# Kernel tuning notes

Measured on AMD Instinct MI355X. Metric: run time of the kernel, lower is better.

Reference implementation:

```python
import jax, jax.numpy as jnp
import numpy as np

N, E = 8192, 65536
IN_C, OUT_C, EF = 64, 16, 8
L1, L2 = 48, 32  # in - floor((in-out)/3), in - floor(2*(in-out)/3)


def setup_inputs() -> dict:
    key = jax.random.key(0)
    ks = jax.random.split(key, 10)
    rn = lambda k, shape, s: jax.random.normal(k, shape, dtype=jnp.float32) * s
    return {
        "x": jax.random.normal(ks[0], (N, IN_C), dtype=jnp.float32),
        "edge_index": jax.random.randint(ks[1], (2, E), 0, N, dtype=jnp.int32),
        "edge_attr": jax.random.normal(ks[2], (E, EF), dtype=jnp.float32),
        "nn1_w": rn(ks[3], (EF, IN_C * L1), 0.05),
        "nn1_b": jnp.zeros((IN_C * L1,), jnp.float32),
        "root1": rn(ks[4], (IN_C, L1), 0.1),
        "bias1": jnp.zeros((L1,), jnp.float32),
        "nn2_w": rn(ks[5], (EF, L1 * L2), 0.05),
        "nn2_b": jnp.zeros((L1 * L2,), jnp.float32),
        "root2": rn(ks[6], (L1, L2), 0.1),
        "bias2": jnp.zeros((L2,), jnp.float32),
        "mu_w": rn(ks[7], (L2, OUT_C), 0.1),
        "mu_b": jnp.zeros((OUT_C,), jnp.float32),
        "ls_w": rn(ks[8], (L2, OUT_C), 0.1),
        "ls_b": jnp.zeros((OUT_C,), jnp.float32),
    }


def _nnconv(x, src, dst, edge_attr, nn_w, nn_b, root, bias, c_in, c_out):
    # edge MLP -> per-edge weight matrices [E, c_in, c_out]
    w = (edge_attr @ nn_w + nn_b).reshape(-1, c_in, c_out)
    msg = jnp.einsum('ei,eio->eo', x[src], w)  # gather + per-edge matvec
    agg = jax.ops.segment_sum(msg, dst, num_segments=x.shape[0])  # sum aggregation
    return agg + x @ root + bias  # root transform + bias


def _gcn(x, src, dst, w, b):
    n = x.shape[0]
    # degree over target nodes, including self-loop (edge_weight = 1)
    deg = jax.ops.segment_sum(jnp.ones_like(src, jnp.float32), dst, num_segments=n) + 1.0
    dinv = jax.lax.rsqrt(deg)
    h = x @ w
    norm = dinv[src] * dinv[dst]  # [E]
    agg = jax.ops.segment_sum(h[src] * norm[:, None], dst, num_segments=n)
    return agg + h * (1.0 / deg)[:, None] + b  # self-loop contribution: deg_i^{-1}


def reference(x, edge_index, edge_attr, nn1_w, nn1_b, root1, bias1,
              nn2_w, nn2_b, root2, bias2, mu_w, mu_b, ls_w, ls_b):
    src, dst = edge_index[0], edge_index[1]
    h = jax.nn.relu(_nnconv(x, src, dst, edge_attr, nn1_w, nn1_b, root1, bias1, IN_C, L1))
    h = jax.nn.relu(_nnconv(h, src, dst, edge_attr, nn2_w, nn2_b, root2, bias2, L1, L2))
    return (_gcn(h, src, dst, mu_w, mu_b), _gcn(h, src, dst, ls_w, ls_b))
```

## Files before the change

kernel.cpp:

```cpp
#include <hip/hip_runtime.h>

#define NN 8192
#define EE 65536
#define IN_C 64
#define L1C 48
#define L2C 32
#define OUT_C 16
#define EF 8

#define T1_COLS 480
#define T2_COLS 320

__global__ __launch_bounds__(256) void k_T1(const float* __restrict__ x,
                                            const float* __restrict__ w,
                                            const float* __restrict__ b,
                                            const float* __restrict__ root,
                                            float* __restrict__ T1) {
    __shared__ float xsT[64 * 16];
    const int n0 = blockIdx.x * 16;
    for (int t = threadIdx.x; t < 16 * 64; t += 256) {
        int n = t >> 6, i = t & 63;
        xsT[i * 16 + n] = x[(n0 + n) * 64 + i];
    }
    __syncthreads();
    for (int c = threadIdx.x; c < T1_COLS; c += 256) {
        int f = c / 48, o = c - f * 48;
        const float* wp;
        if (f < 8)      wp = w + f * 3072 + o;
        else if (f == 8) wp = b + o;
        else             wp = root + o;
        float acc[16];
#pragma unroll
        for (int n = 0; n < 16; n++) acc[n] = 0.f;
#pragma unroll 16
        for (int i = 0; i < 64; i++) {
            float wv = wp[i * 48];
            const float* xr = &xsT[i * 16];
#pragma unroll
            for (int n = 0; n < 16; n++) acc[n] += xr[n] * wv;
        }
#pragma unroll
        for (int n = 0; n < 16; n++) T1[(size_t)(n0 + n) * T1_COLS + c] = acc[n];
    }
}

__global__ __launch_bounds__(256) void k_T2(const float* __restrict__ h1,
                                            const float* __restrict__ w,
                                            const float* __restrict__ b,
                                            const float* __restrict__ root,
                                            float* __restrict__ T2) {
    __shared__ float xsT[48 * 16];
    const int n0 = blockIdx.x * 16;
    for (int t = threadIdx.x; t < 16 * 48; t += 256) {
        int n = t / 48, i = t - n * 48;
        xsT[i * 16 + n] = h1[(n0 + n) * 48 + i];
    }
    __syncthreads();
    for (int c = threadIdx.x; c < T2_COLS; c += 256) {
        int f = c >> 5, o = c & 31;
        const float* wp;
        if (f < 8)      wp = w + f * 1536 + o;
        else if (f == 8) wp = b + o;
        else             wp = root + o;
        float acc[16];
#pragma unroll
        for (int n = 0; n < 16; n++) acc[n] = 0.f;
#pragma unroll 16
        for (int i = 0; i < 48; i++) {
            float wv = wp[i * 32];
            const float* xr = &xsT[i * 16];
#pragma unroll
            for (int n = 0; n < 16; n++) acc[n] += xr[n] * wv;
        }
#pragma unroll
        for (int n = 0; n < 16; n++) T2[(size_t)(n0 + n) * T2_COLS + c] = acc[n];
    }
}

__global__ __launch_bounds__(256) void k_zero(float* __restrict__ p, int n4) {
    int i = blockIdx.x * 256 + threadIdx.x;
    if (i < n4) ((float4*)p)[i] = make_float4(0.f, 0.f, 0.f, 0.f);
}

__global__ __launch_bounds__(256) void k_count(const int* __restrict__ ei,
                                               int* __restrict__ cnt) {
    int e = blockIdx.x * 256 + threadIdx.x;
    if (e < EE) atomicAdd(&cnt[ei[EE + e]], 1);
}

__global__ __launch_bounds__(256) void k_scan(const int* __restrict__ cnt,
                                              int* __restrict__ rowstart,
                                              int* __restrict__ cursor) {
    __shared__ int part[256];
    const int t = threadIdx.x;
    const int base = t * 32;
    int local[32];
    int sum = 0;
#pragma unroll
    for (int k = 0; k < 32; k++) { local[k] = cnt[base + k]; sum += local[k]; }
    part[t] = sum;
    __syncthreads();
    if (t == 0) {
        int run = 0;
        for (int i = 0; i < 256; i++) { int c = part[i]; part[i] = run; run += c; }
    }
    __syncthreads();
    int run = part[t];
#pragma unroll
    for (int k = 0; k < 32; k++) {
        rowstart[base + k] = run;
        cursor[base + k] = run;
        run += local[k];
    }
    if (t == 255) rowstart[8192] = run;
}

__global__ __launch_bounds__(256) void k_scatter(const int* __restrict__ ei,
                                                 int* __restrict__ cursor,
                                                 int* __restrict__ ssrc,
                                                 int* __restrict__ seid) {
    int e = blockIdx.x * 256 + threadIdx.x;
    if (e >= EE) return;
    int d = ei[EE + e];
    int pos = atomicAdd(&cursor[d], 1);
    ssrc[pos] = ei[e];
    seid[pos] = e;
}

__global__ __launch_bounds__(256) void k_agg1(const int* __restrict__ rowstart,
                                              const int* __restrict__ ssrc,
                                              const int* __restrict__ seid,
                                              const float* __restrict__ ea,
                                              const float* __restrict__ T1,
                                              const float* __restrict__ bias1,
                                              float* __restrict__ h1) {
    int idx = blockIdx.x * 256 + threadIdx.x;
    int n = idx / 48, o = idx - n * 48;
    if (n >= NN) return;
    const int rs = rowstart[n], re = rowstart[n + 1];
    float m = 0.f;
    for (int j = rs; j < re; ++j) {
        int s = ssrc[j], eid = seid[j];
        const float* t = T1 + (size_t)s * T1_COLS + o;
        const float4* a4 = (const float4*)(ea + (size_t)eid * 8);
        float4 a0 = a4[0], a1 = a4[1];
        float acc = t[384];
        acc += a0.x * t[0 * 48];
        acc += a0.y * t[1 * 48];
        acc += a0.z * t[2 * 48];
        acc += a0.w * t[3 * 48];
        acc += a1.x * t[4 * 48];
        acc += a1.y * t[5 * 48];
        acc += a1.z * t[6 * 48];
        acc += a1.w * t[7 * 48];
        m += acc;
    }
    float v = m + T1[(size_t)n * T1_COLS + 432 + o] + bias1[o];
    h1[(size_t)n * 48 + o] = v > 0.f ? v : 0.f;
}

__global__ __launch_bounds__(256) void k_agg2(const int* __restrict__ rowstart,
                                              const int* __restrict__ ssrc,
                                              const int* __restrict__ seid,
                                              const float* __restrict__ ea,
                                              const float* __restrict__ T2,
                                              const float* __restrict__ bias2,
                                              const float* __restrict__ mu_w,
                                              const float* __restrict__ mu_b,
                                              const float* __restrict__ ls_w,
                                              const float* __restrict__ ls_b,
                                              float* __restrict__ hmu,
                                              float* __restrict__ hls,
                                              float* __restrict__ dinv,
                                              float* __restrict__ out) {
    __shared__ float h2s[8][32];
    const int n0 = blockIdx.x * 8;
    const int lid = threadIdx.x >> 5;
    const int o = threadIdx.x & 31;
    const int n = n0 + lid;
    const int rs = rowstart[n], re = rowstart[n + 1];
    float m = 0.f;
    for (int j = rs; j < re; ++j) {
        int s = ssrc[j], eid = seid[j];
        const float* t = T2 + (size_t)s * T2_COLS + o;
        const float4* a4 = (const float4*)(ea + (size_t)eid * 8);
        float4 a0 = a4[0], a1 = a4[1];
        float acc = t[256];
        acc += a0.x * t[0 * 32];
        acc += a0.y * t[1 * 32];
        acc += a0.z * t[2 * 32];
        acc += a0.w * t[3 * 32];
        acc += a1.x * t[4 * 32];
        acc += a1.y * t[5 * 32];
        acc += a1.z * t[6 * 32];
        acc += a1.w * t[7 * 32];
        m += acc;
    }
    float v = m + T2[(size_t)n * T2_COLS + 288 + o] + bias2[o];
    h2s[lid][o] = v > 0.f ? v : 0.f;
    __syncthreads();
    const float* wm = (o < 16) ? mu_w : ls_w;
    const float* bb = (o < 16) ? mu_b : ls_b;
    const int oo = o & 15;
    float acc = 0.f;
#pragma unroll
    for (int i = 0; i < 32; i++) acc += h2s[lid][i] * wm[i * 16 + oo];
    float d = (float)(re - rs) + 1.0f;
    float di = rsqrtf(d);
    if (o == 0) dinv[n] = di;
    float init = acc / d + bb[oo];
    if (o < 16) {
        hmu[(size_t)n * 16 + oo] = acc;
        out[(size_t)n * 16 + oo] = init;
    } else {
        hls[(size_t)n * 16 + oo] = acc;
        out[(size_t)NN * 16 + (size_t)n * 16 + oo] = init;
    }
}

__global__ __launch_bounds__(256) void k_gcn(const int* __restrict__ rowstart,
                                             const int* __restrict__ ssrc,
                                             const float* __restrict__ hmu,
                                             const float* __restrict__ hls,
                                             const float* __restrict__ dinv,
                                             float* __restrict__ out) {
    int idx = blockIdx.x * 256 + threadIdx.x;
    int d = idx >> 4, o = idx & 15;
    if (d >= NN) return;
    const int rs = rowstart[d], re = rowstart[d + 1];
    float accm = 0.f, accl = 0.f;
    for (int j = rs; j < re; ++j) {
        int s = ssrc[j];
        float ds_ = dinv[s];
        accm += hmu[(size_t)s * 16 + o] * ds_;
        accl += hls[(size_t)s * 16 + o] * ds_;
    }
    float did = dinv[d];
    out[(size_t)d * 16 + o] += accm * did;
    out[(size_t)NN * 16 + (size_t)d * 16 + o] += accl * did;
}

extern "C" void kernel_launch(void* const* d_in, const int* in_sizes, int n_in,
                              void* d_out, int out_size, void* d_ws, size_t ws_size,
                              hipStream_t stream) {
    const float* x     = (const float*)d_in[0];
    const int*   ei    = (const int*)d_in[1];
    const float* ea    = (const float*)d_in[2];
    const float* nn1_w = (const float*)d_in[3];
    const float* nn1_b = (const float*)d_in[4];
    const float* root1 = (const float*)d_in[5];
    const float* bias1 = (const float*)d_in[6];
    const float* nn2_w = (const float*)d_in[7];
    const float* nn2_b = (const float*)d_in[8];
    const float* root2 = (const float*)d_in[9];
    const float* bias2 = (const float*)d_in[10];
    const float* mu_w  = (const float*)d_in[11];
    const float* mu_b  = (const float*)d_in[12];
    const float* ls_w  = (const float*)d_in[13];
    const float* ls_b  = (const float*)d_in[14];
    float* out = (float*)d_out;

    float* W    = (float*)d_ws;
    float* T1   = W;
    float* T2   = W;
    float* h1   = W + 3932160;
    float* hmu  = h1 + 393216;
    float* hls  = hmu + 131072;
    float* dinv = hls + 131072;
    int* cnt      = (int*)(dinv + 8192);
    int* rowstart = cnt + 8192;
    int* cursor   = rowstart + 8193;
    int* ssrc     = cursor + 8192;
    int* seid     = ssrc + 65536;

    k_zero<<<dim3(8), dim3(256), 0, stream>>>((float*)cnt, 2048);
    k_count<<<dim3(EE / 256), dim3(256), 0, stream>>>(ei, cnt);
    k_T1<<<dim3(NN / 16), dim3(256), 0, stream>>>(x, nn1_w, nn1_b, root1, T1);
    k_scan<<<dim3(1), dim3(256), 0, stream>>>(cnt, rowstart, cursor);
    k_scatter<<<dim3(EE / 256), dim3(256), 0, stream>>>(ei, cursor, ssrc, seid);
    k_agg1<<<dim3((NN * 48 + 255) / 256), dim3(256), 0, stream>>>(
        rowstart, ssrc, seid, ea, T1, bias1, h1);
    k_T2<<<dim3(NN / 16), dim3(256), 0, stream>>>(h1, nn2_w, nn2_b, root2, T2);
    k_agg2<<<dim3(NN / 8), dim3(256), 0, stream>>>(
        rowstart, ssrc, seid, ea, T2, bias2, mu_w, mu_b, ls_w, ls_b,
        hmu, hls, dinv, out);
    k_gcn<<<dim3((NN * 16) / 256), dim3(256), 0, stream>>>(
        rowstart, ssrc, hmu, hls, dinv, out);
}
```

Before: 175.2 us.

## Reorder NNConv math: aggregate edge-attr-weighted inputs first, then apply weights

Replaces the per-node transform tables T1/T2 (gathered per edge) with an aggregate-first formulation: each node sums ea_k * x_src over incoming edges into a Z matrix in shared memory, then one small GEMM against nn_w/nn_b/root produces the layer output. Edge attributes are permuted into CSR order during scatter, so aggregation reads them contiguously. The T1 and T2 kernels and their large workspace traffic go away, and the GCN projection is fused into layer 2. In exchange, per-block shared memory grows and the gather loops are serial per node.

```diff
diff --git a/kernel.cpp b/kernel.cpp
--- a/kernel.cpp
+++ b/kernel.cpp
@@ -2,84 +2,12 @@
 
 #define NN 8192
 #define EE 65536
-#define IN_C 64
-#define L1C 48
-#define L2C 32
-#define OUT_C 16
-#define EF 8
-
-#define T1_COLS 480
-#define T2_COLS 320
-
-__global__ __launch_bounds__(256) void k_T1(const float* __restrict__ x,
-                                            const float* __restrict__ w,
-                                            const float* __restrict__ b,
-                                            const float* __restrict__ root,
-                                            float* __restrict__ T1) {
-    __shared__ float xsT[64 * 16];
-    const int n0 = blockIdx.x * 16;
-    for (int t = threadIdx.x; t < 16 * 64; t += 256) {
-        int n = t >> 6, i = t & 63;
-        xsT[i * 16 + n] = x[(n0 + n) * 64 + i];
-    }
-    __syncthreads();
-    for (int c = threadIdx.x; c < T1_COLS; c += 256) {
-        int f = c / 48, o = c - f * 48;
-        const float* wp;
-        if (f < 8)      wp = w + f * 3072 + o;
-        else if (f == 8) wp = b + o;
-        else             wp = root + o;
-        float acc[16];
-#pragma unroll
-        for (int n = 0; n < 16; n++) acc[n] = 0.f;
-#pragma unroll 16
-        for (int i = 0; i < 64; i++) {
-            float wv = wp[i * 48];
-            const float* xr = &xsT[i * 16];
-#pragma unroll
-            for (int n = 0; n < 16; n++) acc[n] += xr[n] * wv;
-        }
-#pragma unroll
-        for (int n = 0; n < 16; n++) T1[(size_t)(n0 + n) * T1_COLS + c] = acc[n];
-    }
-}
-
-__global__ __launch_bounds__(256) void k_T2(const float* __restrict__ h1,
-                                            const float* __restrict__ w,
-                                            const float* __restrict__ b,
-                                            const float* __restrict__ root,
-                                            float* __restrict__ T2) {
-    __shared__ float xsT[48 * 16];
-    const int n0 = blockIdx.x * 16;
-    for (int t = threadIdx.x; t < 16 * 48; t += 256) {
-        int n = t / 48, i = t - n * 48;
-        xsT[i * 16 + n] = h1[(n0 + n) * 48 + i];
-    }
-    __syncthreads();
-    for (int c = threadIdx.x; c < T2_COLS; c += 256) {
-        int f = c >> 5, o = c & 31;
-        const float* wp;
-        if (f < 8)      wp = w + f * 1536 + o;
-        else if (f == 8) wp = b + o;
-        else             wp = root + o;
-        float acc[16];
-#pragma unroll
-        for (int n = 0; n < 16; n++) acc[n] = 0.f;
-#pragma unroll 16
-        for (int i = 0; i < 48; i++) {
-            float wv = wp[i * 32];
-            const float* xr = &xsT[i * 16];
-#pragma unroll
-            for (int n = 0; n < 16; n++) acc[n] += xr[n] * wv;
-        }
-#pragma unroll
-        for (int n = 0; n < 16; n++) T2[(size_t)(n0 + n) * T2_COLS + c] = acc[n];
-    }
-}
-
-__global__ __launch_bounds__(256) void k_zero(float* __restrict__ p, int n4) {
+#define ZSTRIDE 20
+
+
+__global__ __launch_bounds__(256) void k_zero(int* __restrict__ p) {
     int i = blockIdx.x * 256 + threadIdx.x;
-    if (i < n4) ((float4*)p)[i] = make_float4(0.f, 0.f, 0.f, 0.f);
+    ((int4*)p)[i] = make_int4(0, 0, 0, 0);
 }
 
 __global__ __launch_bounds__(256) void k_count(const int* __restrict__ ei,
@@ -112,109 +40,232 @@
         cursor[base + k] = run;
         run += local[k];
     }
-    if (t == 255) rowstart[8192] = run;
+    if (t == 255) rowstart[NN] = run;
 }
 
 __global__ __launch_bounds__(256) void k_scatter(const int* __restrict__ ei,
+                                                 const float* __restrict__ ea,
                                                  int* __restrict__ cursor,
                                                  int* __restrict__ ssrc,
-                                                 int* __restrict__ seid) {
+                                                 float* __restrict__ sea) {
     int e = blockIdx.x * 256 + threadIdx.x;
     if (e >= EE) return;
-    int d = ei[EE + e];
+    int s = ei[e], d = ei[EE + e];
     int pos = atomicAdd(&cursor[d], 1);
-    ssrc[pos] = ei[e];
-    seid[pos] = e;
-}
-
-__global__ __launch_bounds__(256) void k_agg1(const int* __restrict__ rowstart,
-                                              const int* __restrict__ ssrc,
-                                              const int* __restrict__ seid,
-                                              const float* __restrict__ ea,
-                                              const float* __restrict__ T1,
-                                              const float* __restrict__ bias1,
-                                              float* __restrict__ h1) {
-    int idx = blockIdx.x * 256 + threadIdx.x;
-    int n = idx / 48, o = idx - n * 48;
-    if (n >= NN) return;
-    const int rs = rowstart[n], re = rowstart[n + 1];
-    float m = 0.f;
-    for (int j = rs; j < re; ++j) {
-        int s = ssrc[j], eid = seid[j];
-        const float* t = T1 + (size_t)s * T1_COLS + o;
-        const float4* a4 = (const float4*)(ea + (size_t)eid * 8);
-        float4 a0 = a4[0], a1 = a4[1];
-        float acc = t[384];
-        acc += a0.x * t[0 * 48];
-        acc += a0.y * t[1 * 48];
-        acc += a0.z * t[2 * 48];
-        acc += a0.w * t[3 * 48];
-        acc += a1.x * t[4 * 48];
-        acc += a1.y * t[5 * 48];
-        acc += a1.z * t[6 * 48];
-        acc += a1.w * t[7 * 48];
-        m += acc;
-    }
-    float v = m + T1[(size_t)n * T1_COLS + 432 + o] + bias1[o];
-    h1[(size_t)n * 48 + o] = v > 0.f ? v : 0.f;
-}
-
-__global__ __launch_bounds__(256) void k_agg2(const int* __restrict__ rowstart,
-                                              const int* __restrict__ ssrc,
-                                              const int* __restrict__ seid,
-                                              const float* __restrict__ ea,
-                                              const float* __restrict__ T2,
-                                              const float* __restrict__ bias2,
-                                              const float* __restrict__ mu_w,
-                                              const float* __restrict__ mu_b,
-                                              const float* __restrict__ ls_w,
-                                              const float* __restrict__ ls_b,
-                                              float* __restrict__ hmu,
-                                              float* __restrict__ hls,
-                                              float* __restrict__ dinv,
-                                              float* __restrict__ out) {
-    __shared__ float h2s[8][32];
-    const int n0 = blockIdx.x * 8;
-    const int lid = threadIdx.x >> 5;
-    const int o = threadIdx.x & 31;
-    const int n = n0 + lid;
-    const int rs = rowstart[n], re = rowstart[n + 1];
-    float m = 0.f;
-    for (int j = rs; j < re; ++j) {
-        int s = ssrc[j], eid = seid[j];
-        const float* t = T2 + (size_t)s * T2_COLS + o;
-        const float4* a4 = (const float4*)(ea + (size_t)eid * 8);
-        float4 a0 = a4[0], a1 = a4[1];
-        float acc = t[256];
-        acc += a0.x * t[0 * 32];
-        acc += a0.y * t[1 * 32];
-        acc += a0.z * t[2 * 32];
-        acc += a0.w * t[3 * 32];
-        acc += a1.x * t[4 * 32];
-        acc += a1.y * t[5 * 32];
-        acc += a1.z * t[6 * 32];
-        acc += a1.w * t[7 * 32];
-        m += acc;
-    }
-    float v = m + T2[(size_t)n * T2_COLS + 288 + o] + bias2[o];
-    h2s[lid][o] = v > 0.f ? v : 0.f;
-    __syncthreads();
-    const float* wm = (o < 16) ? mu_w : ls_w;
-    const float* bb = (o < 16) ? mu_b : ls_b;
-    const int oo = o & 15;
-    float acc = 0.f;
+    ssrc[pos] = s;
+    const float4* a = (const float4*)(ea + (size_t)e * 8);
+    float4* bp = (float4*)(sea + (size_t)pos * 8);
+    bp[0] = a[0];
+    bp[1] = a[1];
+}
+
+__global__ __launch_bounds__(256) void k_L1(const int* __restrict__ rowstart,
+                                            const int* __restrict__ ssrc,
+                                            const float* __restrict__ sea,
+                                            const float* __restrict__ x,
+                                            const float* __restrict__ nn1_w,
+                                            const float* __restrict__ nn1_b,
+                                            const float* __restrict__ root1,
+                                            const float* __restrict__ bias1,
+                                            float* __restrict__ h1) {
+    __shared__ __align__(16) float Zt[640 * ZSTRIDE];
+    __shared__ float pacc[4 * 48 * 16];
+    const int n0 = blockIdx.x * 16;
+    {
+        const int g = threadIdx.x >> 6;
+        const int i = threadIdx.x & 63;
+        for (int nb = 0; nb < 16; nb += 4) {
+            const int nn = nb + g;
+            const int n = n0 + nn;
+            const int rs = rowstart[n], re = rowstart[n + 1];
+            float a0 = 0, a1 = 0, a2 = 0, a3 = 0, a4 = 0, a5 = 0, a6 = 0, a7 = 0, as = 0;
+            for (int j = rs; j < re; ++j) {
+                int s = ssrc[j];
+                float xv = x[(size_t)s * 64 + i];
+                const float4* q4 = (const float4*)(sea + (size_t)j * 8);
+                float4 e0 = q4[0], e1 = q4[1];
+                a0 += e0.x * xv; a1 += e0.y * xv; a2 += e0.z * xv; a3 += e0.w * xv;
+                a4 += e1.x * xv; a5 += e1.y * xv; a6 += e1.z * xv; a7 += e1.w * xv;
+                as += xv;
+            }
+            Zt[(0 * 64 + i) * ZSTRIDE + nn] = a0;
+            Zt[(1 * 64 + i) * ZSTRIDE + nn] = a1;
+            Zt[(2 * 64 + i) * ZSTRIDE + nn] = a2;
+            Zt[(3 * 64 + i) * ZSTRIDE + nn] = a3;
+            Zt[(4 * 64 + i) * ZSTRIDE + nn] = a4;
+            Zt[(5 * 64 + i) * ZSTRIDE + nn] = a5;
+            Zt[(6 * 64 + i) * ZSTRIDE + nn] = a6;
+            Zt[(7 * 64 + i) * ZSTRIDE + nn] = a7;
+            Zt[(512 + i) * ZSTRIDE + nn] = as;
+            Zt[(576 + i) * ZSTRIDE + nn] = x[(size_t)n * 64 + i];
+        }
+    }
+    __syncthreads();
+    {
+        const int o = threadIdx.x & 15;
+        const int q = (threadIdx.x >> 4) & 3;
+        const int ks = threadIdx.x >> 6;
+        const int k0 = ks * 160, k1 = k0 + 160;
+        float4 c0 = {0, 0, 0, 0}, c1 = {0, 0, 0, 0}, c2 = {0, 0, 0, 0};
+        const int zb = q * 4;
+        int ka1 = k1 < 512 ? k1 : 512;
+        for (int k = k0; k < ka1; ++k) {
+            const float* wp = nn1_w + k * 48 + o;
+            float w0 = wp[0], w1 = wp[16], w2 = wp[32];
+            float4 z = *(const float4*)&Zt[k * ZSTRIDE + zb];
+            c0.x += z.x * w0; c0.y += z.y * w0; c0.z += z.z * w0; c0.w += z.w * w0;
+            c1.x += z.x * w1; c1.y += z.y * w1; c1.z += z.z * w1; c1.w += z.w * w1;
+            c2.x += z.x * w2; c2.y += z.y * w2; c2.z += z.z * w2; c2.w += z.w * w2;
+        }
+        int kb0 = k0 > 512 ? k0 : 512, kb1 = k1 < 576 ? k1 : 576;
+        for (int k = kb0; k < kb1; ++k) {
+            const float* wp = nn1_b + (k - 512) * 48 + o;
+            float w0 = wp[0], w1 = wp[16], w2 = wp[32];
+            float4 z = *(const float4*)&Zt[k * ZSTRIDE + zb];
+            c0.x += z.x * w0; c0.y += z.y * w0; c0.z += z.z * w0; c0.w += z.w * w0;
+            c1.x += z.x * w1; c1.y += z.y * w1; c1.z += z.z * w1; c1.w += z.w * w1;
+            c2.x += z.x * w2; c2.y += z.y * w2; c2.z += z.z * w2; c2.w += z.w * w2;
+        }
+        int kc0 = k0 > 576 ? k0 : 576;
+        for (int k = kc0; k < k1; ++k) {
+            const float* wp = root1 + (k - 576) * 48 + o;
+            float w0 = wp[0], w1 = wp[16], w2 = wp[32];
+            float4 z = *(const float4*)&Zt[k * ZSTRIDE + zb];
+            c0.x += z.x * w0; c0.y += z.y * w0; c0.z += z.z * w0; c0.w += z.w * w0;
+            c1.x += z.x * w1; c1.y += z.y * w1; c1.z += z.z * w1; c1.w += z.w * w1;
+            c2.x += z.x * w2; c2.y += z.y * w2; c2.z += z.z * w2; c2.w += z.w * w2;
+        }
+        float* pp = pacc + (ks * 48 + o) * 16 + zb;
+        pp[0] = c0.x; pp[1] = c0.y; pp[2] = c0.z; pp[3] = c0.w;
+        pp = pacc + (ks * 48 + o + 16) * 16 + zb;
+        pp[0] = c1.x; pp[1] = c1.y; pp[2] = c1.z; pp[3] = c1.w;
+        pp = pacc + (ks * 48 + o + 32) * 16 + zb;
+        pp[0] = c2.x; pp[1] = c2.y; pp[2] = c2.z; pp[3] = c2.w;
+    }
+    __syncthreads();
+    for (int r = threadIdx.x; r < 768; r += 256) {
+        int o = r >> 4, n = r & 15;
+        float v = pacc[(0 * 48 + o) * 16 + n] + pacc[(1 * 48 + o) * 16 + n] +
+                  pacc[(2 * 48 + o) * 16 + n] + pacc[(3 * 48 + o) * 16 + n] + bias1[o];
+        h1[(size_t)(n0 + n) * 48 + o] = v > 0.f ? v : 0.f;
+    }
+}
+
+__global__ __launch_bounds__(256) void k_L2(const int* __restrict__ rowstart,
+                                            const int* __restrict__ ssrc,
+                                            const float* __restrict__ sea,
+                                            const float* __restrict__ h1,
+                                            const float* __restrict__ nn2_w,
+                                            const float* __restrict__ nn2_b,
+                                            const float* __restrict__ root2,
+                                            const float* __restrict__ bias2,
+                                            const float* __restrict__ mu_w,
+                                            const float* __restrict__ mu_b,
+                                            const float* __restrict__ ls_w,
+                                            const float* __restrict__ ls_b,
+                                            const int* __restrict__ cnt,
+                                            float* __restrict__ hmu,
+                                            float* __restrict__ hls,
+                                            float* __restrict__ dinv,
+                                            float* __restrict__ out) {
+    __shared__ __align__(16) float Zt[480 * ZSTRIDE];
+    __shared__ float pacc[4 * 32 * 16];
+    __shared__ float h2s[16 * 33];
+    const int n0 = blockIdx.x * 16;
+    {
+        const int g = threadIdx.x >> 6;
+        const int i = threadIdx.x & 63;
+        for (int nb = 0; nb < 16; nb += 4) {
+            const int nn = nb + g;
+            const int n = n0 + nn;
+            if (i < 48) {
+                const int rs = rowstart[n], re = rowstart[n + 1];
+                float a0 = 0, a1 = 0, a2 = 0, a3 = 0, a4 = 0, a5 = 0, a6 = 0, a7 = 0, as = 0;
+                for (int j = rs; j < re; ++j) {
+                    int s = ssrc[j];
+                    float hv = h1[(size_t)s * 48 + i];
+                    const float4* q4 = (const float4*)(sea + (size_t)j * 8);
+                    float4 e0 = q4[0], e1 = q4[1];
+                    a0 += e0.x * hv; a1 += e0.y * hv; a2 += e0.z * hv; a3 += e0.w * hv;
+                    a4 += e1.x * hv; a5 += e1.y * hv; a6 += e1.z * hv; a7 += e1.w * hv;
+                    as += hv;
+                }
+                Zt[(0 * 48 + i) * ZSTRIDE + nn] = a0;
+                Zt[(1 * 48 + i) * ZSTRIDE + nn] = a1;
+                Zt[(2 * 48 + i) * ZSTRIDE + nn] = a2;
+                Zt[(3 * 48 + i) * ZSTRIDE + nn] = a3;
+                Zt[(4 * 48 + i) * ZSTRIDE + nn] = a4;
+                Zt[(5 * 48 + i) * ZSTRIDE + nn] = a5;
+                Zt[(6 * 48 + i) * ZSTRIDE + nn] = a6;
+                Zt[(7 * 48 + i) * ZSTRIDE + nn] = a7;
+                Zt[(384 + i) * ZSTRIDE + nn] = as;
+                Zt[(432 + i) * ZSTRIDE + nn] = h1[(size_t)n * 48 + i];
+            }
+        }
+    }
+    __syncthreads();
+    {
+        const int o = threadIdx.x & 15;
+        const int q = (threadIdx.x >> 4) & 3;
+        const int ks = threadIdx.x >> 6;
+        const int k0 = ks * 120, k1 = k0 + 120;
+        float4 c0 = {0, 0, 0, 0}, c1 = {0, 0, 0, 0};
+        const int zb = q * 4;
+        int ka1 = k1 < 384 ? k1 : 384;
+        for (int k = k0; k < ka1; ++k) {
+            const float* wp = nn2_w + k * 32 + o;
+            float w0 = wp[0], w1 = wp[16];
+            float4 z = *(const float4*)&Zt[k * ZSTRIDE + zb];
+            c0.x += z.x * w0; c0.y += z.y * w0; c0.z += z.z * w0; c0.w += z.w * w0;
+            c1.x += z.x * w1; c1.y += z.y * w1; c1.z += z.z * w1; c1.w += z.w * w1;
+        }
+        int kb0 = k0 > 384 ? k0 : 384, kb1 = k1 < 432 ? k1 : 432;
+        for (int k = kb0; k < kb1; ++k) {
+            const float* wp = nn2_b + (k - 384) * 32 + o;
+            float w0 = wp[0], w1 = wp[16];
+            float4 z = *(const float4*)&Zt[k * ZSTRIDE + zb];
+            c0.x += z.x * w0; c0.y += z.y * w0; c0.z += z.z * w0; c0.w += z.w * w0;
+            c1.x += z.x * w1; c1.y += z.y * w1; c1.z += z.z * w1; c1.w += z.w * w1;
+        }
+        int kc0 = k0 > 432 ? k0 : 432;
+        for (int k = kc0; k < k1; ++k) {
+            const float* wp = root2 + (k - 432) * 32 + o;
+            float w0 = wp[0], w1 = wp[16];
+            float4 z = *(const float4*)&Zt[k * ZSTRIDE + zb];
+            c0.x += z.x * w0; c0.y += z.y * w0; c0.z += z.z * w0; c0.w += z.w * w0;
+            c1.x += z.x * w1; c1.y += z.y * w1; c1.z += z.z * w1; c1.w += z.w * w1;
+        }
+        float* pp = pacc + (ks * 32 + o) * 16 + zb;
+        pp[0] = c0.x; pp[1] = c0.y; pp[2] = c0.z; pp[3] = c0.w;
+        pp = pacc + (ks * 32 + o + 16) * 16 + zb;
+        pp[0] = c1.x; pp[1] = c1.y; pp[2] = c1.z; pp[3] = c1.w;
+    }
+    __syncthreads();
+    for (int r = threadIdx.x; r < 512; r += 256) {
+        int o = r >> 4, n = r & 15;
+        float v = pacc[(0 * 32 + o) * 16 + n] + pacc[(1 * 32 + o) * 16 + n] +
+                  pacc[(2 * 32 + o) * 16 + n] + pacc[(3 * 32 + o) * 16 + n] + bias2[o];
+        h2s[n * 33 + o] = v > 0.f ? v : 0.f;
+    }
+    __syncthreads();
+    {
+        const int n = threadIdx.x >> 4;
+        const int o = threadIdx.x & 15;
+        const int gn = n0 + n;
+        float am = 0.f, al = 0.f;
 #pragma unroll
-    for (int i = 0; i < 32; i++) acc += h2s[lid][i] * wm[i * 16 + oo];
-    float d = (float)(re - rs) + 1.0f;
-    float di = rsqrtf(d);
-    if (o == 0) dinv[n] = di;
-    float init = acc / d + bb[oo];
-    if (o < 16) {
-        hmu[(size_t)n * 16 + oo] = acc;
-        out[(size_t)n * 16 + oo] = init;
-    } else {
-        hls[(size_t)n * 16 + oo] = acc;
-        out[(size_t)NN * 16 + (size_t)n * 16 + oo] = init;
+        for (int i = 0; i < 32; i++) {
+            float hv = h2s[n * 33 + i];
+            am += hv * mu_w[i * 16 + o];
+            al += hv * ls_w[i * 16 + o];
+        }
+        float d = (float)cnt[gn] + 1.0f;
+        float di = rsqrtf(d);
+        if (o == 0) dinv[gn] = di;
+        hmu[(size_t)gn * 16 + o] = am;
+        hls[(size_t)gn * 16 + o] = al;
+        out[(size_t)gn * 16 + o] = am / d + mu_b[o];
+        out[(size_t)NN * 16 + (size_t)gn * 16 + o] = al / d + ls_b[o];
     }
 }
 
@@ -226,18 +277,17 @@
                                              float* __restrict__ out) {
     int idx = blockIdx.x * 256 + threadIdx.x;
     int d = idx >> 4, o = idx & 15;
-    if (d >= NN) return;
     const int rs = rowstart[d], re = rowstart[d + 1];
-    float accm = 0.f, accl = 0.f;
+    float am = 0.f, al = 0.f;
     for (int j = rs; j < re; ++j) {
         int s = ssrc[j];
         float ds_ = dinv[s];
-        accm += hmu[(size_t)s * 16 + o] * ds_;
-        accl += hls[(size_t)s * 16 + o] * ds_;
-    }
-    float did = dinv[d];
-    out[(size_t)d * 16 + o] += accm * did;
-    out[(size_t)NN * 16 + (size_t)d * 16 + o] += accl * did;
+        am += hmu[(size_t)s * 16 + o] * ds_;
+        al += hls[(size_t)s * 16 + o] * ds_;
+    }
+    float dd = dinv[d];
+    out[(size_t)d * 16 + o] += am * dd;
+    out[(size_t)NN * 16 + (size_t)d * 16 + o] += al * dd;
 }
 
 extern "C" void kernel_launch(void* const* d_in, const int* in_sizes, int n_in,
@@ -261,9 +311,8 @@
     float* out = (float*)d_out;
 
     float* W    = (float*)d_ws;
-    float* T1   = W;
-    float* T2   = W;
-    float* h1   = W + 3932160;
+    float* sea  = W;
+    float* h1   = sea + 524288;
     float* hmu  = h1 + 393216;
     float* hls  = hmu + 131072;
     float* dinv = hls + 131072;
@@ -271,19 +320,17 @@
     int* rowstart = cnt + 8192;
     int* cursor   = rowstart + 8193;
     int* ssrc     = cursor + 8192;
-    int* seid     = ssrc + 65536;
-
-    k_zero<<<dim3(8), dim3(256), 0, stream>>>((float*)cnt, 2048);
+
+    k_zero<<<dim3(8), dim3(256), 0, stream>>>(cnt);
     k_count<<<dim3(EE / 256), dim3(256), 0, stream>>>(ei, cnt);
-    k_T1<<<dim3(NN / 16), dim3(256), 0, stream>>>(x, nn1_w, nn1_b, root1, T1);
     k_scan<<<dim3(1), dim3(256), 0, stream>>>(cnt, rowstart, cursor);
-    k_scatter<<<dim3(EE / 256), dim3(256), 0, stream>>>(ei, cursor, ssrc, seid);
-    k_agg1<<<dim3((NN * 48 + 255) / 256), dim3(256), 0, stream>>>(
-        rowstart, ssrc, seid, ea, T1, bias1, h1);
-    k_T2<<<dim3(NN / 16), dim3(256), 0, stream>>>(h1, nn2_w, nn2_b, root2, T2);
-    k_agg2<<<dim3(NN / 8), dim3(256), 0, stream>>>(
-        rowstart, ssrc, seid, ea, T2, bias2, mu_w, mu_b, ls_w, ls_b,
-        hmu, hls, dinv, out);
-    k_gcn<<<dim3((NN * 16) / 256), dim3(256), 0, stream>>>(
-        rowstart, ssrc, hmu, hls, dinv, out);
-}
+    k_scatter<<<dim3(EE / 256), dim3(256), 0, stream>>>(ei, ea, cursor, ssrc, sea);
+    k_L1<<<dim3(NN / 16), dim3(256), 0, stream>>>(rowstart, ssrc, sea, x,
+                                                  nn1_w, nn1_b, root1, bias1, h1);
+    k_L2<<<dim3(NN / 16), dim3(256), 0, stream>>>(rowstart, ssrc, sea, h1,
+                                                  nn2_w, nn2_b, root2, bias2,
+                                                  mu_w, mu_b, ls_w, ls_b, cnt,
+                                                  hmu, hls, dinv, out);
+    k_gcn<<<dim3((NN * 16) / 256), dim3(256), 0, stream>>>(rowstart, ssrc,
+                                                           hmu, hls, dinv, out);
+}
```

Result: slower. 225.0 us (+28.5%).
